# Performance work log

Hardware: AMD Instinct MI355X
Metric: run time of the kernel (lower is better)

Reference implementation:

```python
import jax, jax.numpy as jnp
import numpy as np

NUM_NODES = 100000
NODE_FEAT_DIM = 512
EDGE_FEAT_DIM = 512
MEM_DIM = NODE_FEAT_DIM + EDGE_FEAT_DIM  # 1024
BATCH = 65536


def setup_inputs() -> dict:
    key = jax.random.key(0)
    k_ids, k_mem, k_emb, kq, ks, kk = jax.random.split(key, 6)
    scale = 1.0 / np.sqrt(MEM_DIM)
    inp = {
        "node_ids": jax.random.randint(k_ids, (BATCH,), 0, NUM_NODES, dtype=jnp.int64)
        if jax.config.jax_enable_x64 else
        jax.random.randint(k_ids, (BATCH,), 0, NUM_NODES, dtype=jnp.int32),
        # memory bank: (N, 1, D); randomized (instead of the zero init) so math is non-trivial
        "node_memories": jax.random.normal(k_mem, (NUM_NODES, 1, MEM_DIM), dtype=jnp.float32) * 0.02,
        "node_embedding": jax.random.normal(k_emb, (NUM_NODES, MEM_DIM), dtype=jnp.float32) * 0.02,
        "Wq": jax.random.normal(jax.random.fold_in(kq, 0), (MEM_DIM, NODE_FEAT_DIM), dtype=jnp.float32) * scale,
        "bq": jnp.zeros((NODE_FEAT_DIM,), dtype=jnp.float32),
        "Ws": jax.random.normal(jax.random.fold_in(ks, 0), (MEM_DIM, NODE_FEAT_DIM), dtype=jnp.float32) * scale,
        "bs": jnp.zeros((NODE_FEAT_DIM,), dtype=jnp.float32),
        "Wk": jax.random.normal(jax.random.fold_in(kk, 0), (MEM_DIM, NODE_FEAT_DIM), dtype=jnp.float32) * scale,
        "bk": jnp.zeros((NODE_FEAT_DIM,), dtype=jnp.float32),
    }
    return inp


def reference(node_ids, node_memories, node_embedding, Wq, bq, Ws, bs, Wk, bk):
    ids = node_ids.astype(jnp.int32)
    # torch.sum(node_memories[ids], dim=2): reduces feature dim -> (B, 1)
    mem_sum = jnp.sum(node_memories[ids], axis=2)          # (B, 1)
    x = mem_sum + node_embedding[ids]                      # broadcast -> (B, D)
    q = jax.nn.sigmoid(x @ Wq + bq)                        # (B, node_feat_dim)
    s = jax.nn.sigmoid(x @ Ws + bs)
    k = jax.nn.sigmoid(x @ Wk + bk)
    return (q, s, k)
```

## Files before the change

kernel.cpp:

```cpp
#include <hip/hip_runtime.h>
#include <hip/hip_bf16.h>
#include <stdint.h>

#define BATCH_N 65536
#define KDIM 1024
#define NTOT 1536

typedef __bf16 bf16x8 __attribute__((ext_vector_type(8)));
typedef float f32x4 __attribute__((ext_vector_type(4)));

__device__ __forceinline__ unsigned short f2bf(float f) {
    unsigned u = __builtin_bit_cast(unsigned, f);
    u += 0x7FFFu + ((u >> 16) & 1u);
    return (unsigned short)(u >> 16);
}

__global__ __launch_bounds__(256) void prep_kernel(
    const int* __restrict__ ids,
    const float* __restrict__ mem,
    const float* __restrict__ emb,
    unsigned short* __restrict__ x)
{
    const int b = blockIdx.x;
    const int t = threadIdx.x;
    const int id = ids[b];
    const float4* m4 = (const float4*)(mem + (size_t)id * KDIM);
    const float4* e4 = (const float4*)(emb + (size_t)id * KDIM);
    float4 v = m4[t];
    float s = v.x + v.y + v.z + v.w;
    #pragma unroll
    for (int off = 32; off >= 1; off >>= 1) s += __shfl_down(s, off, 64);
    __shared__ float wsum[4];
    const int lane = t & 63, w = t >> 6;
    if (lane == 0) wsum[w] = s;
    __syncthreads();
    const float tot = wsum[0] + wsum[1] + wsum[2] + wsum[3];
    float4 e = e4[t];
    ushort4 o;
    o.x = f2bf(tot + e.x);
    o.y = f2bf(tot + e.y);
    o.z = f2bf(tot + e.z);
    o.w = f2bf(tot + e.w);
    const int k   = t * 4;
    const int ksw = k ^ ((b & 7) << 3);
    *(ushort4*)(x + (size_t)b * KDIM + ksw) = o;
}

__global__ __launch_bounds__(256) void wconv_kernel(
    const float* __restrict__ Wq, const float* __restrict__ Ws,
    const float* __restrict__ Wk, unsigned short* __restrict__ wt)
{
    const int gt = blockIdx.x * 256 + threadIdx.x;
    const int n  = gt % NTOT;
    const int kb = (gt / NTOT) * 4;
    const float* W = (n < 512) ? Wq : ((n < 1024) ? Ws : Wk);
    const int nn = n & 511;
    ushort4 o;
    o.x = f2bf(W[(size_t)(kb + 0) * 512 + nn]);
    o.y = f2bf(W[(size_t)(kb + 1) * 512 + nn]);
    o.z = f2bf(W[(size_t)(kb + 2) * 512 + nn]);
    o.w = f2bf(W[(size_t)(kb + 3) * 512 + nn]);
    const int ksw = kb ^ ((n & 7) << 3);
    *(ushort4*)(wt + (size_t)n * KDIM + ksw) = o;
}

#define BM 256
#define BN 256
#define BK 64
#define MT (BATCH_N / BM)
#define NT (NTOT / BN)
#define NWG (MT * NT)

#define BAR() asm volatile("s_barrier" ::: "memory")
#define LGKM0() asm volatile("s_waitcnt lgkmcnt(0)" ::: "memory")
#define VM2() asm volatile("s_waitcnt vmcnt(2)" ::: "memory")
#define VM0() asm volatile("s_waitcnt vmcnt(0)" ::: "memory")
#define AS1 __attribute__((address_space(1)))
#define AS3 __attribute__((address_space(3)))

__global__ __launch_bounds__(512, 2) void gemm_kernel(
    const unsigned short* __restrict__ X,
    const unsigned short* __restrict__ Wt,
    const float* __restrict__ bq, const float* __restrict__ bs,
    const float* __restrict__ bk, float* __restrict__ out)
{
    __shared__ __align__(16) unsigned short sA[32768];
    __shared__ __align__(16) unsigned short sB[32768];

    const int tid  = threadIdx.x;
    const int xcd  = blockIdx.x & 7;
    const int idx  = blockIdx.x >> 3;
    const int wgid = xcd * (NWG / 8) + idx;
    const int nt   = wgid % NT;
    const int mt   = wgid / NT;
    const int m0   = mt * BM;
    const int n0   = nt * BN;
    const int wid  = tid >> 6;
    const int lane = tid & 63;
    const int wm   = wid >> 2;
    const int wn   = wid & 3;
    const int r16  = lane & 15;
    const int kb0  = (lane >> 4) << 4;
    const int ksw  = (r16 & 7) << 4;

    f32x4 acc[8][4];
    #pragma unroll
    for (int i = 0; i < 8; i++)
        #pragma unroll
        for (int j = 0; j < 4; j++)
            acc[i][j] = f32x4{0.f, 0.f, 0.f, 0.f};

    bf16x8 af[4][2], bfr[2][2];

    const unsigned short* gA = X  + (size_t)(m0 + (tid >> 3)) * KDIM + (tid & 7) * 8;
    const unsigned short* gB = Wt + (size_t)(n0 + (tid >> 3)) * KDIM + (tid & 7) * 8;
    const int ldst = (tid & 448) * 8;

#define STAGE_A(slot, h, kt) do {                                               \
    _Pragma("unroll")                                                            \
    for (int c = 0; c < 2; ++c)                                                  \
        __builtin_amdgcn_global_load_lds(                                        \
            (const AS1 void*)(gA + (size_t)((h) * 128 + c * 64) * KDIM + (kt) * BK), \
            (AS3 void*)(&sA[((slot) * 2 + (h)) * 8192 + c * 4096 + ldst]),       \
            16, 0, 0);                                                           \
} while (0)
#define STAGE_B(slot, h, kt) do {                                               \
    _Pragma("unroll")                                                            \
    for (int c = 0; c < 2; ++c)                                                  \
        __builtin_amdgcn_global_load_lds(                                        \
            (const AS1 void*)(gB + (size_t)((h) * 128 + c * 64) * KDIM + (kt) * BK), \
            (AS3 void*)(&sB[((slot) * 2 + (h)) * 8192 + c * 4096 + ldst]),       \
            16, 0, 0);                                                           \
} while (0)

#define LDA(slot, qa) do {                                                      \
    const char* p = (const char*)&sA[((slot) * 2 + (qa)) * 8192];                \
    _Pragma("unroll")                                                            \
    for (int i = 0; i < 4; ++i)                                                  \
        _Pragma("unroll")                                                        \
        for (int kk = 0; kk < 2; ++kk)                                           \
            af[i][kk] = *(const bf16x8*)(p + (wm * 64 + i * 16 + r16) * 128      \
                                           + ((kk * 64 + kb0) ^ ksw));           \
} while (0)
#define LDB(slot, qb) do {                                                      \
    const char* p = (const char*)&sB[((slot) * 2 + (qb)) * 8192];                \
    _Pragma("unroll")                                                            \
    for (int j = 0; j < 2; ++j)                                                  \
        _Pragma("unroll")                                                        \
        for (int kk = 0; kk < 2; ++kk)                                           \
            bfr[j][kk] = *(const bf16x8*)(p + (wn * 32 + j * 16 + r16) * 128     \
                                            + ((kk * 64 + kb0) ^ ksw));          \
} while (0)

#define MM(QA, QB) do {                                                         \
    __builtin_amdgcn_s_setprio(1);                                               \
    _Pragma("unroll")                                                            \
    for (int i = 0; i < 4; ++i)                                                  \
        _Pragma("unroll")                                                        \
        for (int j = 0; j < 2; ++j)                                              \
            _Pragma("unroll")                                                    \
            for (int kk = 0; kk < 2; ++kk)                                       \
                acc[(QA) * 4 + i][(QB) * 2 + j] =                                \
                    __builtin_amdgcn_mfma_f32_16x16x32_bf16(                     \
                        af[i][kk], bfr[j][kk], acc[(QA) * 4 + i][(QB) * 2 + j],  \
                        0, 0, 0);                                                \
    __builtin_amdgcn_s_setprio(0);                                               \
} while (0)

#define PH(QA, QB, LOADS, STAGES, WAIT) do {                                    \
    LOADS; STAGES; BAR(); LGKM0(); MM(QA, QB); WAIT; BAR();                      \
} while (0)

    STAGE_A(0, 0, 0); STAGE_A(0, 1, 0); STAGE_B(0, 0, 0); STAGE_B(0, 1, 0);
    STAGE_A(1, 0, 1);
    VM2();
    BAR();

    #pragma unroll 1
    for (int t = 0; t < 7; ++t) {
        const int ka = 2 * t + 1, kb2 = 2 * t + 2, kc = 2 * t + 3;
        PH(0, 0, ({ LDA(0, 0); LDB(0, 0); }), STAGE_A(1, 1, ka), (void)0);
        PH(0, 1, LDB(0, 1),                   STAGE_B(1, 0, ka), (void)0);
        PH(1, 1, LDA(0, 1),                   STAGE_B(1, 1, ka), (void)0);
        PH(1, 0, LDB(0, 0),                   STAGE_A(0, 0, kb2), VM2());
        PH(0, 0, ({ LDA(1, 0); LDB(1, 0); }), STAGE_A(0, 1, kb2), (void)0);
        PH(0, 1, LDB(1, 1),                   STAGE_B(0, 0, kb2), (void)0);
        PH(1, 1, LDA(1, 1),                   STAGE_B(0, 1, kb2), (void)0);
        PH(1, 0, LDB(1, 0),                   STAGE_A(1, 0, kc),  VM2());
    }
    PH(0, 0, ({ LDA(0, 0); LDB(0, 0); }), STAGE_A(1, 1, 15), (void)0);
    PH(0, 1, LDB(0, 1),                   STAGE_B(1, 0, 15), (void)0);
    PH(1, 1, LDA(0, 1),                   STAGE_B(1, 1, 15), (void)0);
    PH(1, 0, LDB(0, 0),                   (void)0,           VM0());
    PH(0, 0, ({ LDA(1, 0); LDB(1, 0); }), (void)0,           (void)0);
    PH(0, 1, LDB(1, 1),                   (void)0,           (void)0);
    PH(1, 1, LDA(1, 1),                   (void)0,           (void)0);
    PH(1, 0, LDB(1, 0),                   (void)0,           (void)0);

    const int grp = nt >> 1;
    const float* bias = (grp == 0) ? bq : ((grp == 1) ? bs : bk);
    float* obase = out + (size_t)grp * ((size_t)BATCH_N * 512);
    const int cb = (nt & 1) * 256;
    #pragma unroll
    for (int qb = 0; qb < 2; ++qb)
        #pragma unroll
        for (int j = 0; j < 2; ++j) {
            const int col = cb + qb * 128 + wn * 32 + j * 16 + r16;
            const float bv = bias[col];
            #pragma unroll
            for (int qa = 0; qa < 2; ++qa)
                #pragma unroll
                for (int i = 0; i < 4; ++i) {
                    const int rbase = m0 + qa * 128 + wm * 64 + i * 16 + ((lane >> 4) << 2);
                    #pragma unroll
                    for (int r = 0; r < 4; ++r) {
                        float v = acc[qa * 4 + i][qb * 2 + j][r] + bv;
                        v = 1.0f / (1.0f + __expf(-v));
                        __builtin_nontemporal_store(v, &obase[(size_t)(rbase + r) * 512 + col]);
                    }
                }
        }
#undef STAGE_A
#undef STAGE_B
#undef LDA
#undef LDB
#undef MM
#undef PH
}

extern "C" void kernel_launch(void* const* d_in, const int* in_sizes, int n_in,
                              void* d_out, int out_size, void* d_ws, size_t ws_size,
                              hipStream_t stream) {
    const int*   ids = (const int*)d_in[0];
    const float* mem = (const float*)d_in[1];
    const float* emb = (const float*)d_in[2];
    const float* Wq  = (const float*)d_in[3];
    const float* bq  = (const float*)d_in[4];
    const float* Ws  = (const float*)d_in[5];
    const float* bs  = (const float*)d_in[6];
    const float* Wk  = (const float*)d_in[7];
    const float* bk  = (const float*)d_in[8];
    float* out = (float*)d_out;

    unsigned short* x  = (unsigned short*)d_ws;
    unsigned short* wt = x + (size_t)BATCH_N * KDIM;

    hipLaunchKernelGGL(wconv_kernel, dim3(NTOT), dim3(256), 0, stream, Wq, Ws, Wk, wt);
    hipLaunchKernelGGL(prep_kernel, dim3(BATCH_N), dim3(256), 0, stream, ids, mem, emb, x);
    hipLaunchKernelGGL(gemm_kernel, dim3(NWG), dim3(512), 0, stream,
                       x, wt, bq, bs, bk, out);
}
```

Measured before the change: 421.0 us.

## Restructure GEMM main loop into two-phase pipeline and use wave-per-row prep

The GEMM main loop changes from eight quarter-tile phases per two K-steps to two half-tile phases per K-step. Each wave now holds a 64-column B fragment (bfr[4][2]), so LDS B reads happen once per K-step and the number of barriers drops. LDS reads for the next phase are issued after the MFMAs so they overlap compute, and the explicit lgkmcnt waits are removed. The prep kernel now gives one wave to each batch row with an xor-shuffle reduction, which removes the shared-memory block reduction and __syncthreads. In exchange this uses more registers per wave and depends on a more delicate vmcnt/barrier ordering.

```diff
diff --git a/kernel.cpp b/kernel.cpp
--- a/kernel.cpp
+++ b/kernel.cpp
@@ -21,29 +21,32 @@
     const float* __restrict__ emb,
     unsigned short* __restrict__ x)
 {
-    const int b = blockIdx.x;
-    const int t = threadIdx.x;
-    const int id = ids[b];
-    const float4* m4 = (const float4*)(mem + (size_t)id * KDIM);
-    const float4* e4 = (const float4*)(emb + (size_t)id * KDIM);
-    float4 v = m4[t];
-    float s = v.x + v.y + v.z + v.w;
-    #pragma unroll
-    for (int off = 32; off >= 1; off >>= 1) s += __shfl_down(s, off, 64);
-    __shared__ float wsum[4];
-    const int lane = t & 63, w = t >> 6;
-    if (lane == 0) wsum[w] = s;
-    __syncthreads();
-    const float tot = wsum[0] + wsum[1] + wsum[2] + wsum[3];
-    float4 e = e4[t];
-    ushort4 o;
-    o.x = f2bf(tot + e.x);
-    o.y = f2bf(tot + e.y);
-    o.z = f2bf(tot + e.z);
-    o.w = f2bf(tot + e.w);
-    const int k   = t * 4;
-    const int ksw = k ^ ((b & 7) << 3);
-    *(ushort4*)(x + (size_t)b * KDIM + ksw) = o;
+    const int b    = blockIdx.x * 4 + (threadIdx.x >> 6);
+    const int lane = threadIdx.x & 63;
+    const int id   = ids[b];
+    const float4* m4 = (const float4*)(mem + (size_t)id * KDIM) + lane;
+    const float4* e4 = (const float4*)(emb + (size_t)id * KDIM) + lane;
+    float4 v0 = m4[0];
+    float4 v1 = m4[64];
+    float4 v2 = m4[128];
+    float4 v3 = m4[192];
+    float s = (v0.x + v0.y + v0.z + v0.w) + (v1.x + v1.y + v1.z + v1.w)
+            + (v2.x + v2.y + v2.z + v2.w) + (v3.x + v3.y + v3.z + v3.w);
+    #pragma unroll
+    for (int off = 1; off < 64; off <<= 1) s += __shfl_xor(s, off, 64);
+    unsigned short* xb = x + (size_t)b * KDIM;
+    #pragma unroll
+    for (int q = 0; q < 4; ++q) {
+        float4 e = e4[q * 64];
+        ushort4 o;
+        o.x = f2bf(s + e.x);
+        o.y = f2bf(s + e.y);
+        o.z = f2bf(s + e.z);
+        o.w = f2bf(s + e.w);
+        const int k   = q * 256 + lane * 4;
+        const int ksw = k ^ ((b & 7) << 3);
+        *(ushort4*)(xb + ksw) = o;
+    }
 }
 
 __global__ __launch_bounds__(256) void wconv_kernel(
@@ -72,8 +75,7 @@
 #define NWG (MT * NT)
 
 #define BAR() asm volatile("s_barrier" ::: "memory")
-#define LGKM0() asm volatile("s_waitcnt lgkmcnt(0)" ::: "memory")
-#define VM2() asm volatile("s_waitcnt vmcnt(2)" ::: "memory")
+#define VM4() asm volatile("s_waitcnt vmcnt(4)" ::: "memory")
 #define VM0() asm volatile("s_waitcnt vmcnt(0)" ::: "memory")
 #define AS1 __attribute__((address_space(1)))
 #define AS3 __attribute__((address_space(3)))
@@ -110,31 +112,35 @@
         for (int j = 0; j < 4; j++)
             acc[i][j] = f32x4{0.f, 0.f, 0.f, 0.f};
 
-    bf16x8 af[4][2], bfr[2][2];
+    bf16x8 af[4][2], bfr[4][2];
 
     const unsigned short* gA = X  + (size_t)(m0 + (tid >> 3)) * KDIM + (tid & 7) * 8;
     const unsigned short* gB = Wt + (size_t)(n0 + (tid >> 3)) * KDIM + (tid & 7) * 8;
     const int ldst = (tid & 448) * 8;
 
-#define STAGE_A(slot, h, kt) do {                                               \
-    _Pragma("unroll")                                                            \
-    for (int c = 0; c < 2; ++c)                                                  \
-        __builtin_amdgcn_global_load_lds(                                        \
-            (const AS1 void*)(gA + (size_t)((h) * 128 + c * 64) * KDIM + (kt) * BK), \
-            (AS3 void*)(&sA[((slot) * 2 + (h)) * 8192 + c * 4096 + ldst]),       \
-            16, 0, 0);                                                           \
-} while (0)
-#define STAGE_B(slot, h, kt) do {                                               \
-    _Pragma("unroll")                                                            \
-    for (int c = 0; c < 2; ++c)                                                  \
-        __builtin_amdgcn_global_load_lds(                                        \
-            (const AS1 void*)(gB + (size_t)((h) * 128 + c * 64) * KDIM + (kt) * BK), \
-            (AS3 void*)(&sB[((slot) * 2 + (h)) * 8192 + c * 4096 + ldst]),       \
-            16, 0, 0);                                                           \
-} while (0)
-
-#define LDA(slot, qa) do {                                                      \
-    const char* p = (const char*)&sA[((slot) * 2 + (qa)) * 8192];                \
+#define STAGE_A(slot, kt) do {                                                  \
+    _Pragma("unroll")                                                            \
+    for (int h = 0; h < 2; ++h)                                                  \
+        _Pragma("unroll")                                                        \
+        for (int c = 0; c < 2; ++c)                                              \
+            __builtin_amdgcn_global_load_lds(                                    \
+                (const AS1 void*)(gA + (size_t)(h * 128 + c * 64) * KDIM + (kt) * BK), \
+                (AS3 void*)(&sA[(slot) * 16384 + h * 8192 + c * 4096 + ldst]),   \
+                16, 0, 0);                                                       \
+} while (0)
+#define STAGE_B(slot, kt) do {                                                  \
+    _Pragma("unroll")                                                            \
+    for (int h = 0; h < 2; ++h)                                                  \
+        _Pragma("unroll")                                                        \
+        for (int c = 0; c < 2; ++c)                                              \
+            __builtin_amdgcn_global_load_lds(                                    \
+                (const AS1 void*)(gB + (size_t)(h * 128 + c * 64) * KDIM + (kt) * BK), \
+                (AS3 void*)(&sB[(slot) * 16384 + h * 8192 + c * 4096 + ldst]),   \
+                16, 0, 0);                                                       \
+} while (0)
+
+#define RD_A(slot, qa) do {                                                     \
+    const char* p = (const char*)&sA[(slot) * 16384 + (qa) * 8192];              \
     _Pragma("unroll")                                                            \
     for (int i = 0; i < 4; ++i)                                                  \
         _Pragma("unroll")                                                        \
@@ -142,90 +148,80 @@
             af[i][kk] = *(const bf16x8*)(p + (wm * 64 + i * 16 + r16) * 128      \
                                            + ((kk * 64 + kb0) ^ ksw));           \
 } while (0)
-#define LDB(slot, qb) do {                                                      \
-    const char* p = (const char*)&sB[((slot) * 2 + (qb)) * 8192];                \
-    _Pragma("unroll")                                                            \
-    for (int j = 0; j < 2; ++j)                                                  \
+#define RD_B(slot) do {                                                         \
+    const char* p = (const char*)&sB[(slot) * 16384 + (wn >> 1) * 8192];         \
+    _Pragma("unroll")                                                            \
+    for (int j = 0; j < 4; ++j)                                                  \
         _Pragma("unroll")                                                        \
         for (int kk = 0; kk < 2; ++kk)                                           \
-            bfr[j][kk] = *(const bf16x8*)(p + (wn * 32 + j * 16 + r16) * 128     \
+            bfr[j][kk] = *(const bf16x8*)(p + ((wn & 1) * 64 + j * 16 + r16) * 128 \
                                             + ((kk * 64 + kb0) ^ ksw));          \
 } while (0)
 
-#define MM(QA, QB) do {                                                         \
+#define MM(QA) do {                                                             \
     __builtin_amdgcn_s_setprio(1);                                               \
     _Pragma("unroll")                                                            \
     for (int i = 0; i < 4; ++i)                                                  \
         _Pragma("unroll")                                                        \
-        for (int j = 0; j < 2; ++j)                                              \
+        for (int j = 0; j < 4; ++j)                                              \
             _Pragma("unroll")                                                    \
             for (int kk = 0; kk < 2; ++kk)                                       \
-                acc[(QA) * 4 + i][(QB) * 2 + j] =                                \
-                    __builtin_amdgcn_mfma_f32_16x16x32_bf16(                     \
-                        af[i][kk], bfr[j][kk], acc[(QA) * 4 + i][(QB) * 2 + j],  \
-                        0, 0, 0);                                                \
+                acc[(QA) * 4 + i][j] = __builtin_amdgcn_mfma_f32_16x16x32_bf16(  \
+                    af[i][kk], bfr[j][kk], acc[(QA) * 4 + i][j], 0, 0, 0);       \
     __builtin_amdgcn_s_setprio(0);                                               \
 } while (0)
 
-#define PH(QA, QB, LOADS, STAGES, WAIT) do {                                    \
-    LOADS; STAGES; BAR(); LGKM0(); MM(QA, QB); WAIT; BAR();                      \
-} while (0)
-
-    STAGE_A(0, 0, 0); STAGE_A(0, 1, 0); STAGE_B(0, 0, 0); STAGE_B(0, 1, 0);
-    STAGE_A(1, 0, 1);
-    VM2();
+    STAGE_A(0, 0); STAGE_B(0, 0); STAGE_A(1, 1);
+    VM4();
     BAR();
+    RD_A(0, 0); RD_B(0);
 
     #pragma unroll 1
-    for (int t = 0; t < 7; ++t) {
-        const int ka = 2 * t + 1, kb2 = 2 * t + 2, kc = 2 * t + 3;
-        PH(0, 0, ({ LDA(0, 0); LDB(0, 0); }), STAGE_A(1, 1, ka), (void)0);
-        PH(0, 1, LDB(0, 1),                   STAGE_B(1, 0, ka), (void)0);
-        PH(1, 1, LDA(0, 1),                   STAGE_B(1, 1, ka), (void)0);
-        PH(1, 0, LDB(0, 0),                   STAGE_A(0, 0, kb2), VM2());
-        PH(0, 0, ({ LDA(1, 0); LDB(1, 0); }), STAGE_A(0, 1, kb2), (void)0);
-        PH(0, 1, LDB(1, 1),                   STAGE_B(0, 0, kb2), (void)0);
-        PH(1, 1, LDA(1, 1),                   STAGE_B(0, 1, kb2), (void)0);
-        PH(1, 0, LDB(1, 0),                   STAGE_A(1, 0, kc),  VM2());
+    for (int t = 0; t < 14; ++t) {
+        const int s = t & 1, s1 = s ^ 1;
+        BAR();
+        MM(0);
+        RD_A(s, 1);
+        STAGE_B(s1, t + 1);
+        BAR();
+        MM(1);
+        STAGE_A(s, t + 2);
+        VM4();
+        BAR();
+        RD_A(s1, 0); RD_B(s1);
     }
-    PH(0, 0, ({ LDA(0, 0); LDB(0, 0); }), STAGE_A(1, 1, 15), (void)0);
-    PH(0, 1, LDB(0, 1),                   STAGE_B(1, 0, 15), (void)0);
-    PH(1, 1, LDA(0, 1),                   STAGE_B(1, 1, 15), (void)0);
-    PH(1, 0, LDB(0, 0),                   (void)0,           VM0());
-    PH(0, 0, ({ LDA(1, 0); LDB(1, 0); }), (void)0,           (void)0);
-    PH(0, 1, LDB(1, 1),                   (void)0,           (void)0);
-    PH(1, 1, LDA(1, 1),                   (void)0,           (void)0);
-    PH(1, 0, LDB(1, 0),                   (void)0,           (void)0);
+    BAR(); MM(0); RD_A(0, 1); STAGE_B(1, 15);
+    BAR(); MM(1); VM0();
+    BAR(); RD_A(1, 0); RD_B(1);
+    BAR(); MM(0); RD_A(1, 1);
+    BAR(); MM(1);
 
     const int grp = nt >> 1;
     const float* bias = (grp == 0) ? bq : ((grp == 1) ? bs : bk);
     float* obase = out + (size_t)grp * ((size_t)BATCH_N * 512);
     const int cb = (nt & 1) * 256;
     #pragma unroll
-    for (int qb = 0; qb < 2; ++qb)
+    for (int j = 0; j < 4; ++j) {
+        const int col = cb + wn * 64 + j * 16 + r16;
+        const float bv = bias[col];
         #pragma unroll
-        for (int j = 0; j < 2; ++j) {
-            const int col = cb + qb * 128 + wn * 32 + j * 16 + r16;
-            const float bv = bias[col];
+        for (int qa = 0; qa < 2; ++qa)
             #pragma unroll
-            for (int qa = 0; qa < 2; ++qa)
+            for (int i = 0; i < 4; ++i) {
+                const int rbase = m0 + qa * 128 + wm * 64 + i * 16 + ((lane >> 4) << 2);
                 #pragma unroll
-                for (int i = 0; i < 4; ++i) {
-                    const int rbase = m0 + qa * 128 + wm * 64 + i * 16 + ((lane >> 4) << 2);
-                    #pragma unroll
-                    for (int r = 0; r < 4; ++r) {
-                        float v = acc[qa * 4 + i][qb * 2 + j][r] + bv;
-                        v = 1.0f / (1.0f + __expf(-v));
-                        __builtin_nontemporal_store(v, &obase[(size_t)(rbase + r) * 512 + col]);
-                    }
+                for (int r = 0; r < 4; ++r) {
+                    float v = acc[qa * 4 + i][j][r] + bv;
+                    v = 1.0f / (1.0f + __expf(-v));
+                    __builtin_nontemporal_store(v, &obase[(size_t)(rbase + r) * 512 + col]);
                 }
-        }
+            }
+    }
 #undef STAGE_A
 #undef STAGE_B
-#undef LDA
-#undef LDB
+#undef RD_A
+#undef RD_B
 #undef MM
-#undef PH
 }
 
 extern "C" void kernel_launch(void* const* d_in, const int* in_sizes, int n_in,
@@ -246,7 +242,7 @@
     unsigned short* wt = x + (size_t)BATCH_N * KDIM;
 
     hipLaunchKernelGGL(wconv_kernel, dim3(NTOT), dim3(256), 0, stream, Wq, Ws, Wk, wt);
-    hipLaunchKernelGGL(prep_kernel, dim3(BATCH_N), dim3(256), 0, stream, ids, mem, emb, x);
+    hipLaunchKernelGGL(prep_kernel, dim3(BATCH_N / 4), dim3(256), 0, stream, ids, mem, emb, x);
     hipLaunchKernelGGL(gemm_kernel, dim3(NWG), dim3(512), 0, stream,
                        x, wt, bq, bs, bk, out);
 }
```

Measured after the change: 412.0 us. -2.1%, faster.

## Use wave-per-row gather prep and reschedule GEMM staging with double B fragments

Applied to the files above, without the earlier changes.

The prep kernel now handles one batch row per wavefront, four rows per block, with a xor-shuffle reduction. This removes the shared-memory reduction and the block-wide barrier. The GEMM main loop is restructured: B fragments are kept in two register sets so that reloading B is skipped for some quadrants, and the global-to-LDS staging order and wait counts (vmcnt 6) are reshuffled so more loads stay in flight. This adds register pressure and risks an LDS race if the staging order overwrites buffers that are still being read.

```diff
diff --git a/kernel.cpp b/kernel.cpp
--- a/kernel.cpp
+++ b/kernel.cpp
@@ -21,29 +21,32 @@
     const float* __restrict__ emb,
     unsigned short* __restrict__ x)
 {
-    const int b = blockIdx.x;
-    const int t = threadIdx.x;
-    const int id = ids[b];
-    const float4* m4 = (const float4*)(mem + (size_t)id * KDIM);
-    const float4* e4 = (const float4*)(emb + (size_t)id * KDIM);
-    float4 v = m4[t];
-    float s = v.x + v.y + v.z + v.w;
-    #pragma unroll
-    for (int off = 32; off >= 1; off >>= 1) s += __shfl_down(s, off, 64);
-    __shared__ float wsum[4];
-    const int lane = t & 63, w = t >> 6;
-    if (lane == 0) wsum[w] = s;
-    __syncthreads();
-    const float tot = wsum[0] + wsum[1] + wsum[2] + wsum[3];
-    float4 e = e4[t];
-    ushort4 o;
-    o.x = f2bf(tot + e.x);
-    o.y = f2bf(tot + e.y);
-    o.z = f2bf(tot + e.z);
-    o.w = f2bf(tot + e.w);
-    const int k   = t * 4;
-    const int ksw = k ^ ((b & 7) << 3);
-    *(ushort4*)(x + (size_t)b * KDIM + ksw) = o;
+    const int b    = blockIdx.x * 4 + (threadIdx.x >> 6);
+    const int lane = threadIdx.x & 63;
+    const int id   = ids[b];
+    const float4* m4 = (const float4*)(mem + (size_t)id * KDIM) + lane;
+    const float4* e4 = (const float4*)(emb + (size_t)id * KDIM) + lane;
+    float4 v0 = m4[0];
+    float4 v1 = m4[64];
+    float4 v2 = m4[128];
+    float4 v3 = m4[192];
+    float s = (v0.x + v0.y + v0.z + v0.w) + (v1.x + v1.y + v1.z + v1.w)
+            + (v2.x + v2.y + v2.z + v2.w) + (v3.x + v3.y + v3.z + v3.w);
+    #pragma unroll
+    for (int off = 1; off < 64; off <<= 1) s += __shfl_xor(s, off, 64);
+    unsigned short* xb = x + (size_t)b * KDIM;
+    #pragma unroll
+    for (int q = 0; q < 4; ++q) {
+        float4 e = e4[q * 64];
+        ushort4 o;
+        o.x = f2bf(s + e.x);
+        o.y = f2bf(s + e.y);
+        o.z = f2bf(s + e.z);
+        o.w = f2bf(s + e.w);
+        const int k   = q * 256 + lane * 4;
+        const int ksw = k ^ ((b & 7) << 3);
+        *(ushort4*)(xb + ksw) = o;
+    }
 }
 
 __global__ __launch_bounds__(256) void wconv_kernel(
@@ -73,7 +76,7 @@
 
 #define BAR() asm volatile("s_barrier" ::: "memory")
 #define LGKM0() asm volatile("s_waitcnt lgkmcnt(0)" ::: "memory")
-#define VM2() asm volatile("s_waitcnt vmcnt(2)" ::: "memory")
+#define VM6() asm volatile("s_waitcnt vmcnt(6)" ::: "memory")
 #define VM0() asm volatile("s_waitcnt vmcnt(0)" ::: "memory")
 #define AS1 __attribute__((address_space(1)))
 #define AS3 __attribute__((address_space(3)))
@@ -110,13 +113,13 @@
         for (int j = 0; j < 4; j++)
             acc[i][j] = f32x4{0.f, 0.f, 0.f, 0.f};
 
-    bf16x8 af[4][2], bfr[2][2];
+    bf16x8 af[4][2], bfr0[2][2], bfr1[2][2];
 
     const unsigned short* gA = X  + (size_t)(m0 + (tid >> 3)) * KDIM + (tid & 7) * 8;
     const unsigned short* gB = Wt + (size_t)(n0 + (tid >> 3)) * KDIM + (tid & 7) * 8;
     const int ldst = (tid & 448) * 8;
 
-#define STAGE_A(slot, h, kt) do {                                               \
+#define STG_A(slot, h, kt) do {                                                 \
     _Pragma("unroll")                                                            \
     for (int c = 0; c < 2; ++c)                                                  \
         __builtin_amdgcn_global_load_lds(                                        \
@@ -124,7 +127,7 @@
             (AS3 void*)(&sA[((slot) * 2 + (h)) * 8192 + c * 4096 + ldst]),       \
             16, 0, 0);                                                           \
 } while (0)
-#define STAGE_B(slot, h, kt) do {                                               \
+#define STG_B(slot, h, kt) do {                                                 \
     _Pragma("unroll")                                                            \
     for (int c = 0; c < 2; ++c)                                                  \
         __builtin_amdgcn_global_load_lds(                                        \
@@ -142,17 +145,17 @@
             af[i][kk] = *(const bf16x8*)(p + (wm * 64 + i * 16 + r16) * 128      \
                                            + ((kk * 64 + kb0) ^ ksw));           \
 } while (0)
-#define LDB(slot, qb) do {                                                      \
+#define LDB(slot, qb, SET) do {                                                 \
     const char* p = (const char*)&sB[((slot) * 2 + (qb)) * 8192];                \
     _Pragma("unroll")                                                            \
     for (int j = 0; j < 2; ++j)                                                  \
         _Pragma("unroll")                                                        \
         for (int kk = 0; kk < 2; ++kk)                                           \
-            bfr[j][kk] = *(const bf16x8*)(p + (wn * 32 + j * 16 + r16) * 128     \
+            SET[j][kk] = *(const bf16x8*)(p + (wn * 32 + j * 16 + r16) * 128     \
                                             + ((kk * 64 + kb0) ^ ksw));          \
 } while (0)
 
-#define MM(QA, QB) do {                                                         \
+#define MM(QA, QB, SET) do {                                                    \
     __builtin_amdgcn_s_setprio(1);                                               \
     _Pragma("unroll")                                                            \
     for (int i = 0; i < 4; ++i)                                                  \
@@ -162,40 +165,50 @@
             for (int kk = 0; kk < 2; ++kk)                                       \
                 acc[(QA) * 4 + i][(QB) * 2 + j] =                                \
                     __builtin_amdgcn_mfma_f32_16x16x32_bf16(                     \
-                        af[i][kk], bfr[j][kk], acc[(QA) * 4 + i][(QB) * 2 + j],  \
+                        af[i][kk], SET[j][kk], acc[(QA) * 4 + i][(QB) * 2 + j],  \
                         0, 0, 0);                                                \
     __builtin_amdgcn_s_setprio(0);                                               \
 } while (0)
 
-#define PH(QA, QB, LOADS, STAGES, WAIT) do {                                    \
-    LOADS; STAGES; BAR(); LGKM0(); MM(QA, QB); WAIT; BAR();                      \
-} while (0)
-
-    STAGE_A(0, 0, 0); STAGE_A(0, 1, 0); STAGE_B(0, 0, 0); STAGE_B(0, 1, 0);
-    STAGE_A(1, 0, 1);
-    VM2();
+    STG_A(0, 0, 0); STG_A(0, 1, 0); STG_B(0, 0, 0); STG_B(0, 1, 0);
+    STG_A(1, 0, 1); STG_B(1, 1, 1); STG_A(1, 1, 1);
+    VM0();
     BAR();
 
     #pragma unroll 1
     for (int t = 0; t < 7; ++t) {
         const int ka = 2 * t + 1, kb2 = 2 * t + 2, kc = 2 * t + 3;
-        PH(0, 0, ({ LDA(0, 0); LDB(0, 0); }), STAGE_A(1, 1, ka), (void)0);
-        PH(0, 1, LDB(0, 1),                   STAGE_B(1, 0, ka), (void)0);
-        PH(1, 1, LDA(0, 1),                   STAGE_B(1, 1, ka), (void)0);
-        PH(1, 0, LDB(0, 0),                   STAGE_A(0, 0, kb2), VM2());
-        PH(0, 0, ({ LDA(1, 0); LDB(1, 0); }), STAGE_A(0, 1, kb2), (void)0);
-        PH(0, 1, LDB(1, 1),                   STAGE_B(0, 0, kb2), (void)0);
-        PH(1, 1, LDA(1, 1),                   STAGE_B(0, 1, kb2), (void)0);
-        PH(1, 0, LDB(1, 0),                   STAGE_A(1, 0, kc),  VM2());
+        LDA(0, 0); LDB(0, 0, bfr0); STG_B(1, 0, ka);
+        BAR(); LGKM0(); MM(0, 0, bfr0); BAR();
+        LDB(0, 1, bfr1); STG_A(0, 0, kb2);
+        BAR(); LGKM0(); MM(0, 1, bfr1); BAR();
+        LDA(0, 1); STG_B(0, 1, kb2);
+        BAR(); LGKM0(); MM(1, 1, bfr1); BAR();
+        STG_A(0, 1, kb2);
+        BAR(); LGKM0(); MM(1, 0, bfr0); VM6(); BAR();
+        LDA(1, 0); LDB(1, 0, bfr0); STG_B(0, 0, kb2);
+        BAR(); LGKM0(); MM(0, 0, bfr0); BAR();
+        LDB(1, 1, bfr1); STG_A(1, 0, kc);
+        BAR(); LGKM0(); MM(0, 1, bfr1); BAR();
+        LDA(1, 1); STG_B(1, 1, kc);
+        BAR(); LGKM0(); MM(1, 1, bfr1); BAR();
+        STG_A(1, 1, kc);
+        BAR(); LGKM0(); MM(1, 0, bfr0); VM6(); BAR();
     }
-    PH(0, 0, ({ LDA(0, 0); LDB(0, 0); }), STAGE_A(1, 1, 15), (void)0);
-    PH(0, 1, LDB(0, 1),                   STAGE_B(1, 0, 15), (void)0);
-    PH(1, 1, LDA(0, 1),                   STAGE_B(1, 1, 15), (void)0);
-    PH(1, 0, LDB(0, 0),                   (void)0,           VM0());
-    PH(0, 0, ({ LDA(1, 0); LDB(1, 0); }), (void)0,           (void)0);
-    PH(0, 1, LDB(1, 1),                   (void)0,           (void)0);
-    PH(1, 1, LDA(1, 1),                   (void)0,           (void)0);
-    PH(1, 0, LDB(1, 0),                   (void)0,           (void)0);
+    LDA(0, 0); LDB(0, 0, bfr0); STG_B(1, 0, 15);
+    BAR(); LGKM0(); MM(0, 0, bfr0); BAR();
+    LDB(0, 1, bfr1);
+    BAR(); LGKM0(); MM(0, 1, bfr1); BAR();
+    LDA(0, 1);
+    BAR(); LGKM0(); MM(1, 1, bfr1); BAR();
+    BAR(); LGKM0(); MM(1, 0, bfr0); VM0(); BAR();
+    LDA(1, 0); LDB(1, 0, bfr0);
+    BAR(); LGKM0(); MM(0, 0, bfr0); BAR();
+    LDB(1, 1, bfr1);
+    BAR(); LGKM0(); MM(0, 1, bfr1); BAR();
+    LDA(1, 1);
+    BAR(); LGKM0(); MM(1, 1, bfr1); BAR();
+    BAR(); LGKM0(); MM(1, 0, bfr0);
 
     const int grp = nt >> 1;
     const float* bias = (grp == 0) ? bq : ((grp == 1) ? bs : bk);
@@ -220,12 +233,11 @@
                     }
                 }
         }
-#undef STAGE_A
-#undef STAGE_B
+#undef STG_A
+#undef STG_B
 #undef LDA
 #undef LDB
 #undef MM
-#undef PH
 }
 
 extern "C" void kernel_launch(void* const* d_in, const int* in_sizes, int n_in,
@@ -246,7 +258,7 @@
     unsigned short* wt = x + (size_t)BATCH_N * KDIM;
 
     hipLaunchKernelGGL(wconv_kernel, dim3(NTOT), dim3(256), 0, stream, Wq, Ws, Wk, wt);
-    hipLaunchKernelGGL(prep_kernel, dim3(BATCH_N), dim3(256), 0, stream, ids, mem, emb, x);
+    hipLaunchKernelGGL(prep_kernel, dim3(BATCH_N / 4), dim3(256), 0, stream, ids, mem, emb, x);
     hipLaunchKernelGGL(gemm_kernel, dim3(NWG), dim3(512), 0, stream,
                        x, wt, bq, bs, bk, out);
 }
```

Measured after the change: 393.2 us. 6.6% less time.
